# Optimization experiments

Measured on AMD Instinct MI355X. Metric: run time of the kernel, lower is better.

Reference implementation:

```python
import jax, jax.numpy as jnp
import numpy as np

N = 50000      # nodes
E = 800000     # edges (avg degree 16)
IN = 128       # input feature dim
H = 128        # hidden dim (all layers output H; out_channels unused in source)
DROP_P = 0.5


def setup_inputs() -> dict:
    key = jax.random.key(0)
    ks = jax.random.split(key, 8)
    s_in = 1.0 / np.sqrt(IN).astype(np.float32)
    s_h = 1.0 / np.sqrt(H).astype(np.float32)
    return {
        "x": jax.random.normal(ks[0], (N, IN), jnp.float32),
        "edge_index": jax.random.randint(ks[1], (2, E), 0, N, dtype=jnp.int32),
        "Wl0": jax.random.normal(ks[2], (H, IN), jnp.float32) * s_in,
        "bl0": jnp.zeros((H,), jnp.float32),
        "Wr0": jax.random.normal(ks[3], (H, IN), jnp.float32) * s_in,
        "Wl1": jax.random.normal(ks[4], (H, H), jnp.float32) * s_h,
        "bl1": jnp.zeros((H,), jnp.float32),
        "Wr1": jax.random.normal(ks[5], (H, H), jnp.float32) * s_h,
    }


def _sage_conv(x, src, dst, Wl, bl, Wr):
    # mean-aggregate neighbor messages: gather x[src], scatter-add to dst
    agg = jax.ops.segment_sum(x[src], dst, num_segments=N)          # [N, D]
    deg = jax.ops.segment_sum(jnp.ones((src.shape[0],), x.dtype), dst,
                              num_segments=N)                        # [N]
    agg = agg / jnp.maximum(deg, 1.0)[:, None]                       # scatter_mean (0 for isolated nodes)
    # PyG SAGEConv: lin_l(agg) (with bias) + lin_r(x) (no bias)
    return agg @ Wl.T + bl + x @ Wr.T


def reference(x, edge_index, Wl0, bl0, Wr0, Wl1, bl1, Wr1):
    src, dst = edge_index[0], edge_index[1]
    h = _sage_conv(x, src, dst, Wl0, bl0, Wr0)
    h = jax.nn.relu(h)
    # dropout(p=0.5, training=True) with a fixed key for determinism
    keep = jax.random.bernoulli(jax.random.key(42), 1.0 - DROP_P, h.shape)
    h = jnp.where(keep, h / (1.0 - DROP_P), 0.0)
    out = _sage_conv(h, src, dst, Wl1, bl1, Wr1)
    return out
```

## Files before the change

### kernel.cpp

```cpp
#include <hip/hip_runtime.h>
#include <hip/hip_bf16.h>


#define HDIM 128
#define KDIM 256
#define NBUK 256
#define BNODE 196
#define BCAP 4096
#define BCH 2048

typedef __attribute__((ext_vector_type(8))) short bshort8;
typedef __attribute__((ext_vector_type(4))) float f32x4;
typedef __attribute__((ext_vector_type(2))) float f32x2;

__device__ __forceinline__ ushort f2b(float f) {
  __hip_bfloat16 h = __float2bfloat16(f);
  return *(ushort*)&h;
}
__device__ __forceinline__ unsigned int pack2(float lo, float hi) {
  return (unsigned int)f2b(lo) | ((unsigned int)f2b(hi) << 16);
}

#if __has_builtin(__builtin_amdgcn_cvt_pk_f32_fp8) && __has_builtin(__builtin_amdgcn_cvt_pk_fp8_f32)
#define FP8_HW 1
#endif

__device__ __forceinline__ unsigned int fp8e1(float f) {
  unsigned int u = __float_as_uint(f);
  unsigned int s = (u >> 24) & 0x80u;
  unsigned int mag = u & 0x7FFFFFFFu;
  if (mag < 0x38800000u) return s;
  if (mag > 0x43E00000u) mag = 0x43E00000u;
  unsigned int r = mag + 0x7FFFFu + ((mag >> 20) & 1u);
  return s | ((r >> 20) - 960u);
}
__device__ __forceinline__ float fp8d1(unsigned int b) {
  unsigned int v = b & 0x7Fu;
  float fn = __uint_as_float(((b & 0x80u) << 24) | ((v + 960u) << 20));
  return v >= 8u ? fn : 0.0f;
}

__device__ __forceinline__ unsigned int fp8x4_enc(float f0, float f1, float f2, float f3) {
#ifdef FP8_HW
  int u = 0;
  u = __builtin_amdgcn_cvt_pk_fp8_f32(f0, f1, u, false);
  u = __builtin_amdgcn_cvt_pk_fp8_f32(f2, f3, u, true);
  return (unsigned int)u;
#else
  return fp8e1(f0) | (fp8e1(f1) << 8) | (fp8e1(f2) << 16) | (fp8e1(f3) << 24);
#endif
}
__device__ __forceinline__ void fp8x4_acc(float* a, unsigned int w) {
#ifdef FP8_HW
  f32x2 lo = __builtin_amdgcn_cvt_pk_f32_fp8((int)w, false);
  f32x2 hi = __builtin_amdgcn_cvt_pk_f32_fp8((int)w, true);
  a[0] += lo.x; a[1] += lo.y; a[2] += hi.x; a[3] += hi.y;
#else
  a[0] += fp8d1(w & 255u); a[1] += fp8d1((w >> 8) & 255u);
  a[2] += fp8d1((w >> 16) & 255u); a[3] += fp8d1(w >> 24);
#endif
}

__device__ __forceinline__ unsigned int tf_rotl(unsigned int x, int d) {
  return (x << d) | (x >> (32 - d));
}
__device__ __forceinline__ bool dropout_keep(unsigned int j) {
  unsigned int x0 = 0u, x1 = j;
  const unsigned int ks0 = 0u, ks1 = 42u, ks2 = 0x1BD11BDAu ^ 0u ^ 42u;
  x0 += ks0; x1 += ks1;
#define TF_R(r) { x0 += x1; x1 = tf_rotl(x1, (r)); x1 ^= x0; }
  TF_R(13) TF_R(15) TF_R(26) TF_R(6)
  x0 += ks1; x1 += ks2 + 1u;
  TF_R(17) TF_R(29) TF_R(16) TF_R(24)
  x0 += ks2; x1 += ks0 + 2u;
  TF_R(13) TF_R(15) TF_R(26) TF_R(6)
  x0 += ks0; x1 += ks1 + 3u;
  TF_R(17) TF_R(29) TF_R(16) TF_R(24)
  x0 += ks1; x1 += ks2 + 4u;
  TF_R(13) TF_R(15) TF_R(26) TF_R(6)
  x0 += ks2; x1 += ks0 + 5u;
#undef TF_R
  unsigned int r = x0 ^ x1;
  float u = __uint_as_float((r >> 9) | 0x3f800000u) - 1.0f;
  return u < 0.5f;
}

__global__ __launch_bounds__(256) void bin_cvt_k(
    const int* __restrict__ src, const int* __restrict__ dst,
    int* __restrict__ bucketCount, unsigned int* __restrict__ pairs, int E, int EB,
    const float* __restrict__ x,
    const float* __restrict__ Wl0, const float* __restrict__ Wr0,
    const float* __restrict__ Wl1, const float* __restrict__ Wr1,
    ushort* __restrict__ Xb, unsigned char* __restrict__ Xq,
    ushort* __restrict__ Wc0, ushort* __restrict__ Wc1, int N) {
  __shared__ int hist[NBUK];
  __shared__ int lofs[NBUK];
  __shared__ int lcur[NBUK];
  __shared__ int gbase[NBUK];
  __shared__ unsigned int ordv[BCH];
  __shared__ unsigned char ordb[BCH];

  int b = blockIdx.x;
  if (b >= EB) {
    b -= EB;
    if (b < 64) {
      int t = b * 256 + threadIdx.x;
      int o = t >> 7, k = t & 127;
      Wc0[o * KDIM + k] = f2b(Wl0[t]);
      Wc0[o * KDIM + HDIM + k] = f2b(Wr0[t]);
      Wc1[o * KDIM + k] = f2b(Wl1[t]);
      Wc1[o * KDIM + HDIM + k] = f2b(Wr1[t]);
    } else {
      int t = (b - 64) * 256 + threadIdx.x;
      if (t < N * 32) {
        int n = t >> 5, c4 = t & 31;
        float4 v = *(const float4*)&x[(size_t)n * HDIM + c4 * 4];
        uint2 p;
        p.x = pack2(v.x, v.y);
        p.y = pack2(v.z, v.w);
        *(uint2*)&Xb[(size_t)n * HDIM + c4 * 4] = p;
        *(unsigned int*)&Xq[(size_t)n * HDIM + c4 * 4] = fp8x4_enc(v.x, v.y, v.z, v.w);
      }
    }
    return;
  }

  hist[threadIdx.x] = 0;
  __syncthreads();
  int begin = b * BCH;
  int n = min(BCH, E - begin);
  unsigned int vals[BCH / 256];
  int bks[BCH / 256];
  int cnt = 0;
  for (int i = threadIdx.x; i < n; i += 256) {
    int s = src[begin + i], d = dst[begin + i];
    int bk = d / BNODE;
    int dloc = d - bk * BNODE;
    vals[cnt] = ((unsigned int)s << 8) | (unsigned int)dloc;
    bks[cnt] = bk;
    ++cnt;
    atomicAdd(&hist[bk], 1);
  }
  __syncthreads();
  {
    int v = hist[threadIdx.x];
    lofs[threadIdx.x] = v;
    __syncthreads();
    for (int off = 1; off < NBUK; off <<= 1) {
      int t = (threadIdx.x >= off) ? lofs[threadIdx.x - off] : 0;
      __syncthreads();
      lofs[threadIdx.x] += t;
      __syncthreads();
    }
    int ex = lofs[threadIdx.x] - v;
    __syncthreads();
    lofs[threadIdx.x] = ex;
    lcur[threadIdx.x] = ex;
    gbase[threadIdx.x] = atomicAdd(&bucketCount[threadIdx.x], v);
  }
  __syncthreads();
  for (int k = 0; k < cnt; ++k) {
    int bk = bks[k];
    int p = atomicAdd(&lcur[bk], 1);
    ordv[p] = vals[k];
    ordb[p] = (unsigned char)bk;
  }
  __syncthreads();
  for (int j = threadIdx.x; j < n; j += 256) {
    int bk = ordb[j];
    pairs[bk * BCAP + gbase[bk] + (j - lofs[bk])] = ordv[j];
  }
}

__global__ __launch_bounds__(256) void build_k(const unsigned int* __restrict__ pairs,
                                               const int* __restrict__ bucketCount,
                                               int* __restrict__ deg,
                                               int* __restrict__ rowptr,
                                               ushort* __restrict__ eidx, int N) {
  __shared__ int h[BNODE];
  __shared__ int lofs[BNODE];
  __shared__ int cur[BNODE];
  const int b = blockIdx.x;
  const int base = b * BCAP;
  const int cnt = bucketCount[b];
  const int nodebase = b * BNODE;
  const int nloc = min(BNODE, N - nodebase);
  if (threadIdx.x < BNODE) h[threadIdx.x] = 0;
  __syncthreads();
  for (int i = threadIdx.x; i < cnt; i += 256) atomicAdd(&h[pairs[base + i] & 255u], 1);
  __syncthreads();
  if (threadIdx.x < BNODE) lofs[threadIdx.x] = h[threadIdx.x];
  __syncthreads();
  for (int off = 1; off < BNODE; off <<= 1) {
    int t = (threadIdx.x >= off && threadIdx.x < BNODE) ? lofs[threadIdx.x - off] : 0;
    __syncthreads();
    if (threadIdx.x < BNODE) lofs[threadIdx.x] += t;
    __syncthreads();
  }
  if (threadIdx.x < BNODE) {
    int ex = lofs[threadIdx.x] - h[threadIdx.x];
    cur[threadIdx.x] = ex;
    if (threadIdx.x < nloc) {
      deg[nodebase + threadIdx.x] = h[threadIdx.x];
      rowptr[nodebase + threadIdx.x] = base + ex;
    }
  }
  __syncthreads();
  for (int i = threadIdx.x; i < cnt; i += 256) {
    unsigned int v = pairs[base + i];
    int pos = atomicAdd(&cur[v & 255u], 1);
    eidx[base + pos] = (ushort)(v >> 8);
  }
}

__global__ __launch_bounds__(256) void agg_p(const unsigned char* __restrict__ Fq,
                                             ushort* __restrict__ Ag,
                                             const ushort* __restrict__ eidx,
                                             const int* __restrict__ rowptr,
                                             const int* __restrict__ deg, int N) {
  const int lane = threadIdx.x & 63;
  const int wv = threadIdx.x >> 6;
  const int n0 = (blockIdx.x * 4 + wv) * 2;
  if (n0 >= N) return;
  const int n1 = n0 + 1;
  const bool has1 = n1 < N;
  const int es = lane >> 3;
  const int cl = lane & 7;
  const int r0 = rowptr[n0];
  const int d0 = deg[n0];
  const int r1 = has1 ? rowptr[n1] : 0;
  const int d1 = has1 ? deg[n1] : 0;
  float a[16], b[16];
#pragma unroll
  for (int i = 0; i < 16; ++i) { a[i] = 0.0f; b[i] = 0.0f; }
  const int dm = max(d0, d1);
  for (int j = 0; j < dm; j += 16) {
    uint4 va[2], vb[2];
    bool ma[2], mb[2];
#pragma unroll
    for (int u = 0; u < 2; ++u) {
      int e = j + u * 8 + es;
      ma[u] = e < d0;
      mb[u] = e < d1;
      if (ma[u]) {
        int s = eidx[r0 + e];
        va[u] = *(const uint4*)&Fq[(size_t)s * HDIM + cl * 16];
      }
      if (mb[u]) {
        int s = eidx[r1 + e];
        vb[u] = *(const uint4*)&Fq[(size_t)s * HDIM + cl * 16];
      }
    }
#pragma unroll
    for (int u = 0; u < 2; ++u) {
      if (ma[u]) {
        fp8x4_acc(&a[0], va[u].x);
        fp8x4_acc(&a[4], va[u].y);
        fp8x4_acc(&a[8], va[u].z);
        fp8x4_acc(&a[12], va[u].w);
      }
      if (mb[u]) {
        fp8x4_acc(&b[0], vb[u].x);
        fp8x4_acc(&b[4], vb[u].y);
        fp8x4_acc(&b[8], vb[u].z);
        fp8x4_acc(&b[12], vb[u].w);
      }
    }
  }
#pragma unroll
  for (int i = 0; i < 16; ++i) {
    a[i] += __shfl_xor(a[i], 8, 64);
    a[i] += __shfl_xor(a[i], 16, 64);
    a[i] += __shfl_xor(a[i], 32, 64);
    b[i] += __shfl_xor(b[i], 8, 64);
    b[i] += __shfl_xor(b[i], 16, 64);
    b[i] += __shfl_xor(b[i], 32, 64);
  }
  if (es == 0) {
    float rd = 1.0f / fmaxf((float)d0, 1.0f);
    uint4 p0, p1;
    p0.x = pack2(a[0] * rd, a[1] * rd);
    p0.y = pack2(a[2] * rd, a[3] * rd);
    p0.z = pack2(a[4] * rd, a[5] * rd);
    p0.w = pack2(a[6] * rd, a[7] * rd);
    p1.x = pack2(a[8] * rd, a[9] * rd);
    p1.y = pack2(a[10] * rd, a[11] * rd);
    p1.z = pack2(a[12] * rd, a[13] * rd);
    p1.w = pack2(a[14] * rd, a[15] * rd);
    *(uint4*)&Ag[(size_t)n0 * HDIM + cl * 16] = p0;
    *(uint4*)&Ag[(size_t)n0 * HDIM + cl * 16 + 8] = p1;
  } else if (es == 1 && has1) {
    float rd = 1.0f / fmaxf((float)d1, 1.0f);
    uint4 p0, p1;
    p0.x = pack2(b[0] * rd, b[1] * rd);
    p0.y = pack2(b[2] * rd, b[3] * rd);
    p0.z = pack2(b[4] * rd, b[5] * rd);
    p0.w = pack2(b[6] * rd, b[7] * rd);
    p1.x = pack2(b[8] * rd, b[9] * rd);
    p1.y = pack2(b[10] * rd, b[11] * rd);
    p1.z = pack2(b[12] * rd, b[13] * rd);
    p1.w = pack2(b[14] * rd, b[15] * rd);
    *(uint4*)&Ag[(size_t)n1 * HDIM + cl * 16] = p0;
    *(uint4*)&Ag[(size_t)n1 * HDIM + cl * 16 + 8] = p1;
  }
}

template <int MODE>
__global__ __launch_bounds__(256) void gemm_mfma(const ushort* __restrict__ Agg,
                                                 const ushort* __restrict__ F,
                                                 const ushort* __restrict__ Wc,
                                                 ushort* __restrict__ hb,
                                                 unsigned char* __restrict__ hq,
                                                 float* __restrict__ fout,
                                                 const float* __restrict__ bias,
                                                 int N) {
  __shared__ char smem[34816];
  ushort* Wl = (ushort*)smem;
  float* Tl = (float*)smem;
  const int tid = threadIdx.x;
  const int lane = tid & 63;
  const int wid = tid >> 6;
  const int quad = lane >> 4;
  const int l15 = lane & 15;
  const int n0 = blockIdx.x * 64;

  int rowA = n0 + wid * 16 + l15;
  if (rowA >= N) rowA = N - 1;
  bshort8 afA[4], afF[4];
#pragma unroll
  for (int ks = 0; ks < 4; ++ks) {
    afA[ks] = *(const bshort8*)&Agg[(size_t)rowA * HDIM + ks * 32 + quad * 8];
    afF[ks] = *(const bshort8*)&F[(size_t)rowA * HDIM + ks * 32 + quad * 8];
  }

  f32x4 acc[8];
#pragma unroll
  for (int i = 0; i < 8; ++i) acc[i] = (f32x4){0.f, 0.f, 0.f, 0.f};

#pragma unroll
  for (int half = 0; half < 2; ++half) {
    __syncthreads();
#pragma unroll
    for (int i = 0; i < 8; ++i) {
      int q = i * 256 + tid;
      int row = q >> 4, seg = q & 15;
      *(uint4*)&Wl[row * 136 + seg * 8] = *(const uint4*)&Wc[row * KDIM + half * HDIM + seg * 8];
    }
    __syncthreads();
#pragma unroll
    for (int ks = 0; ks < 4; ++ks) {
#pragma unroll
      for (int os = 0; os < 8; ++os) {
        bshort8 bf = *(const bshort8*)&Wl[(os * 16 + l15) * 136 + ks * 32 + quad * 8];
        acc[os] = __builtin_amdgcn_mfma_f32_16x16x32_bf16(
            half == 0 ? afA[ks] : afF[ks], bf, acc[os], 0, 0, 0);
      }
    }
  }

  __syncthreads();

  const int wbase = wid * (16 * 132);
#pragma unroll
  for (int os = 0; os < 8; ++os)
#pragma unroll
    for (int r = 0; r < 4; ++r)
      Tl[wbase + (quad * 4 + r) * 132 + os * 16 + l15] = acc[os][r];

  __syncthreads();

#pragma unroll
  for (int i = 0; i < 8; ++i) {
    int q = i * 64 + lane;
    int r = q >> 5;
    int c4 = q & 31;
    int n = n0 + wid * 16 + r;
    if (n >= N) continue;
    int c = c4 * 4;
    float4 v = *(float4*)&Tl[wbase + r * 132 + c];
    const float4 bv = *(const float4*)&bias[c];
    v.x += bv.x; v.y += bv.y; v.z += bv.z; v.w += bv.w;
    if (MODE == 1) {
      v.x = v.x > 0.0f ? v.x : 0.0f;
      v.y = v.y > 0.0f ? v.y : 0.0f;
      v.z = v.z > 0.0f ? v.z : 0.0f;
      v.w = v.w > 0.0f ? v.w : 0.0f;
      unsigned int fj = (unsigned int)n * HDIM + (unsigned int)c;
      v.x = dropout_keep(fj + 0u) ? v.x * 2.0f : 0.0f;
      v.y = dropout_keep(fj + 1u) ? v.y * 2.0f : 0.0f;
      v.z = dropout_keep(fj + 2u) ? v.z * 2.0f : 0.0f;
      v.w = dropout_keep(fj + 3u) ? v.w * 2.0f : 0.0f;
      uint2 p;
      p.x = pack2(v.x, v.y);
      p.y = pack2(v.z, v.w);
      *(uint2*)&hb[(size_t)n * HDIM + c] = p;
      *(unsigned int*)&hq[(size_t)n * HDIM + c] = fp8x4_enc(v.x, v.y, v.z, v.w);
    } else {
      *(float4*)&fout[(size_t)n * HDIM + c] = v;
    }
  }
}

extern "C" void kernel_launch(void* const* d_in, const int* in_sizes, int n_in,
                              void* d_out, int out_size, void* d_ws, size_t ws_size,
                              hipStream_t stream) {
  const float* x   = (const float*)d_in[0];
  const int*   ei  = (const int*)d_in[1];
  const float* Wl0 = (const float*)d_in[2];
  const float* bl0 = (const float*)d_in[3];
  const float* Wr0 = (const float*)d_in[4];
  const float* Wl1 = (const float*)d_in[5];
  const float* bl1 = (const float*)d_in[6];
  const float* Wr1 = (const float*)d_in[7];
  float* out = (float*)d_out;

  const int N = in_sizes[0] / HDIM;
  const int E = in_sizes[1] / 2;
  const int* src = ei;
  const int* dst = ei + E;

  const int Na = (N + 63) & ~63;
  int* bucketCount = (int*)d_ws;
  int* deg         = bucketCount + NBUK;
  int* rowptr      = deg + Na;
  unsigned int* pairs = (unsigned int*)(rowptr + Na);
  ushort* eidx     = (ushort*)(pairs + NBUK * BCAP);
  size_t off = (((size_t)(eidx + NBUK * BCAP) - (size_t)d_ws) + 255) & ~(size_t)255;
  ushort* Wc0 = (ushort*)((char*)d_ws + off);
  ushort* Wc1 = Wc0 + 128 * KDIM;
  ushort* Xb  = Wc1 + 128 * KDIM;
  ushort* Hb  = Xb + (size_t)N * HDIM;
  ushort* Ag  = Hb + (size_t)N * HDIM;
  unsigned char* Xq = (unsigned char*)(Ag + (size_t)N * HDIM);
  unsigned char* Hq = Xq + (size_t)N * HDIM;

  hipMemsetAsync(bucketCount, 0, NBUK * sizeof(int), stream);

  const int EB = (E + BCH - 1) / BCH;
  const int GB = (N + 63) / 64;
  const int AB = (N + 7) / 8;
  const int CB = EB + 64 + (N * 32 + 255) / 256;

  bin_cvt_k<<<CB, 256, 0, stream>>>(src, dst, bucketCount, pairs, E, EB,
                                    x, Wl0, Wr0, Wl1, Wr1, Xb, Xq, Wc0, Wc1, N);
  build_k<<<NBUK, 256, 0, stream>>>(pairs, bucketCount, deg, rowptr, eidx, N);

  agg_p<<<AB, 256, 0, stream>>>(Xq, Ag, eidx, rowptr, deg, N);
  gemm_mfma<1><<<GB, 256, 0, stream>>>(Ag, Xb, Wc0, Hb, Hq, nullptr, bl0, N);
  agg_p<<<AB, 256, 0, stream>>>(Hq, Ag, eidx, rowptr, deg, N);
  gemm_mfma<2><<<GB, 256, 0, stream>>>(Ag, Hb, Wc1, nullptr, nullptr, out, bl1, N);
}
```

Measured before the change: 216.5 us.

## Fuse neighbor aggregation into the MFMA GEMM kernel via shared memory

Merges the gather-mean aggregation kernel into the GEMM kernel. Each block now aggregates its own 64 nodes into LDS as bf16 and feeds the MFMA directly from there, so the global Ag buffer and two kernel launches go away. In exchange, the grid shrinks from N/8 blocks to N/64, so each wave processes 16 nodes serially. The irregular gather loses parallelism and latency hiding, which may hurt the memory-bound aggregation.

```diff
diff --git a/kernel.cpp b/kernel.cpp
--- a/kernel.cpp
+++ b/kernel.cpp
@@ -213,108 +213,19 @@
   }
 }
 
-__global__ __launch_bounds__(256) void agg_p(const unsigned char* __restrict__ Fq,
-                                             ushort* __restrict__ Ag,
-                                             const ushort* __restrict__ eidx,
-                                             const int* __restrict__ rowptr,
-                                             const int* __restrict__ deg, int N) {
-  const int lane = threadIdx.x & 63;
-  const int wv = threadIdx.x >> 6;
-  const int n0 = (blockIdx.x * 4 + wv) * 2;
-  if (n0 >= N) return;
-  const int n1 = n0 + 1;
-  const bool has1 = n1 < N;
-  const int es = lane >> 3;
-  const int cl = lane & 7;
-  const int r0 = rowptr[n0];
-  const int d0 = deg[n0];
-  const int r1 = has1 ? rowptr[n1] : 0;
-  const int d1 = has1 ? deg[n1] : 0;
-  float a[16], b[16];
-#pragma unroll
-  for (int i = 0; i < 16; ++i) { a[i] = 0.0f; b[i] = 0.0f; }
-  const int dm = max(d0, d1);
-  for (int j = 0; j < dm; j += 16) {
-    uint4 va[2], vb[2];
-    bool ma[2], mb[2];
-#pragma unroll
-    for (int u = 0; u < 2; ++u) {
-      int e = j + u * 8 + es;
-      ma[u] = e < d0;
-      mb[u] = e < d1;
-      if (ma[u]) {
-        int s = eidx[r0 + e];
-        va[u] = *(const uint4*)&Fq[(size_t)s * HDIM + cl * 16];
-      }
-      if (mb[u]) {
-        int s = eidx[r1 + e];
-        vb[u] = *(const uint4*)&Fq[(size_t)s * HDIM + cl * 16];
-      }
-    }
-#pragma unroll
-    for (int u = 0; u < 2; ++u) {
-      if (ma[u]) {
-        fp8x4_acc(&a[0], va[u].x);
-        fp8x4_acc(&a[4], va[u].y);
-        fp8x4_acc(&a[8], va[u].z);
-        fp8x4_acc(&a[12], va[u].w);
-      }
-      if (mb[u]) {
-        fp8x4_acc(&b[0], vb[u].x);
-        fp8x4_acc(&b[4], vb[u].y);
-        fp8x4_acc(&b[8], vb[u].z);
-        fp8x4_acc(&b[12], vb[u].w);
-      }
-    }
-  }
-#pragma unroll
-  for (int i = 0; i < 16; ++i) {
-    a[i] += __shfl_xor(a[i], 8, 64);
-    a[i] += __shfl_xor(a[i], 16, 64);
-    a[i] += __shfl_xor(a[i], 32, 64);
-    b[i] += __shfl_xor(b[i], 8, 64);
-    b[i] += __shfl_xor(b[i], 16, 64);
-    b[i] += __shfl_xor(b[i], 32, 64);
-  }
-  if (es == 0) {
-    float rd = 1.0f / fmaxf((float)d0, 1.0f);
-    uint4 p0, p1;
-    p0.x = pack2(a[0] * rd, a[1] * rd);
-    p0.y = pack2(a[2] * rd, a[3] * rd);
-    p0.z = pack2(a[4] * rd, a[5] * rd);
-    p0.w = pack2(a[6] * rd, a[7] * rd);
-    p1.x = pack2(a[8] * rd, a[9] * rd);
-    p1.y = pack2(a[10] * rd, a[11] * rd);
-    p1.z = pack2(a[12] * rd, a[13] * rd);
-    p1.w = pack2(a[14] * rd, a[15] * rd);
-    *(uint4*)&Ag[(size_t)n0 * HDIM + cl * 16] = p0;
-    *(uint4*)&Ag[(size_t)n0 * HDIM + cl * 16 + 8] = p1;
-  } else if (es == 1 && has1) {
-    float rd = 1.0f / fmaxf((float)d1, 1.0f);
-    uint4 p0, p1;
-    p0.x = pack2(b[0] * rd, b[1] * rd);
-    p0.y = pack2(b[2] * rd, b[3] * rd);
-    p0.z = pack2(b[4] * rd, b[5] * rd);
-    p0.w = pack2(b[6] * rd, b[7] * rd);
-    p1.x = pack2(b[8] * rd, b[9] * rd);
-    p1.y = pack2(b[10] * rd, b[11] * rd);
-    p1.z = pack2(b[12] * rd, b[13] * rd);
-    p1.w = pack2(b[14] * rd, b[15] * rd);
-    *(uint4*)&Ag[(size_t)n1 * HDIM + cl * 16] = p0;
-    *(uint4*)&Ag[(size_t)n1 * HDIM + cl * 16 + 8] = p1;
-  }
-}
-
 template <int MODE>
-__global__ __launch_bounds__(256) void gemm_mfma(const ushort* __restrict__ Agg,
-                                                 const ushort* __restrict__ F,
-                                                 const ushort* __restrict__ Wc,
-                                                 ushort* __restrict__ hb,
-                                                 unsigned char* __restrict__ hq,
-                                                 float* __restrict__ fout,
-                                                 const float* __restrict__ bias,
-                                                 int N) {
+__global__ __launch_bounds__(256) void fused_k(const unsigned char* __restrict__ Fq,
+                                               const ushort* __restrict__ F,
+                                               const ushort* __restrict__ Wc,
+                                               ushort* __restrict__ hb,
+                                               unsigned char* __restrict__ hq,
+                                               float* __restrict__ fout,
+                                               const float* __restrict__ bias,
+                                               const ushort* __restrict__ eidx,
+                                               const int* __restrict__ rowptr,
+                                               const int* __restrict__ deg, int N) {
   __shared__ char smem[34816];
+  ushort* AgL = (ushort*)smem;
   ushort* Wl = (ushort*)smem;
   float* Tl = (float*)smem;
   const int tid = threadIdx.x;
@@ -324,14 +235,107 @@
   const int l15 = lane & 15;
   const int n0 = blockIdx.x * 64;
 
-  int rowA = n0 + wid * 16 + l15;
-  if (rowA >= N) rowA = N - 1;
+  {
+    const int es = lane >> 3;
+    const int cl = lane & 7;
+    for (int p = 0; p < 16; p += 2) {
+      const int ln0 = wid * 16 + p;
+      const int ln1 = ln0 + 1;
+      const int na = n0 + ln0;
+      const int nb2 = n0 + ln1;
+      const int r0 = (na < N) ? rowptr[na] : 0;
+      const int d0 = (na < N) ? deg[na] : 0;
+      const int r1 = (nb2 < N) ? rowptr[nb2] : 0;
+      const int d1 = (nb2 < N) ? deg[nb2] : 0;
+      float a[16], b[16];
+#pragma unroll
+      for (int i = 0; i < 16; ++i) { a[i] = 0.0f; b[i] = 0.0f; }
+      const int dm = max(d0, d1);
+      for (int j = 0; j < dm; j += 16) {
+        uint4 va[2], vb[2];
+        bool ma[2], mb[2];
+#pragma unroll
+        for (int u = 0; u < 2; ++u) {
+          int e = j + u * 8 + es;
+          ma[u] = e < d0;
+          mb[u] = e < d1;
+          if (ma[u]) {
+            int s = eidx[r0 + e];
+            va[u] = *(const uint4*)&Fq[(size_t)s * HDIM + cl * 16];
+          }
+          if (mb[u]) {
+            int s = eidx[r1 + e];
+            vb[u] = *(const uint4*)&Fq[(size_t)s * HDIM + cl * 16];
+          }
+        }
+#pragma unroll
+        for (int u = 0; u < 2; ++u) {
+          if (ma[u]) {
+            fp8x4_acc(&a[0], va[u].x);
+            fp8x4_acc(&a[4], va[u].y);
+            fp8x4_acc(&a[8], va[u].z);
+            fp8x4_acc(&a[12], va[u].w);
+          }
+          if (mb[u]) {
+            fp8x4_acc(&b[0], vb[u].x);
+            fp8x4_acc(&b[4], vb[u].y);
+            fp8x4_acc(&b[8], vb[u].z);
+            fp8x4_acc(&b[12], vb[u].w);
+          }
+        }
+      }
+#pragma unroll
+      for (int i = 0; i < 16; ++i) {
+        a[i] += __shfl_xor(a[i], 8, 64);
+        a[i] += __shfl_xor(a[i], 16, 64);
+        a[i] += __shfl_xor(a[i], 32, 64);
+        b[i] += __shfl_xor(b[i], 8, 64);
+        b[i] += __shfl_xor(b[i], 16, 64);
+        b[i] += __shfl_xor(b[i], 32, 64);
+      }
+      if (es == 0) {
+        float rd = 1.0f / fmaxf((float)d0, 1.0f);
+        uint4 p0, p1;
+        p0.x = pack2(a[0] * rd, a[1] * rd);
+        p0.y = pack2(a[2] * rd, a[3] * rd);
+        p0.z = pack2(a[4] * rd, a[5] * rd);
+        p0.w = pack2(a[6] * rd, a[7] * rd);
+        p1.x = pack2(a[8] * rd, a[9] * rd);
+        p1.y = pack2(a[10] * rd, a[11] * rd);
+        p1.z = pack2(a[12] * rd, a[13] * rd);
+        p1.w = pack2(a[14] * rd, a[15] * rd);
+        *(uint4*)&AgL[ln0 * 136 + cl * 16] = p0;
+        *(uint4*)&AgL[ln0 * 136 + cl * 16 + 8] = p1;
+      } else if (es == 1) {
+        float rd = 1.0f / fmaxf((float)d1, 1.0f);
+        uint4 p0, p1;
+        p0.x = pack2(b[0] * rd, b[1] * rd);
+        p0.y = pack2(b[2] * rd, b[3] * rd);
+        p0.z = pack2(b[4] * rd, b[5] * rd);
+        p0.w = pack2(b[6] * rd, b[7] * rd);
+        p1.x = pack2(b[8] * rd, b[9] * rd);
+        p1.y = pack2(b[10] * rd, b[11] * rd);
+        p1.z = pack2(b[12] * rd, b[13] * rd);
+        p1.w = pack2(b[14] * rd, b[15] * rd);
+        *(uint4*)&AgL[ln1 * 136 + cl * 16] = p0;
+        *(uint4*)&AgL[ln1 * 136 + cl * 16 + 8] = p1;
+      }
+    }
+  }
+  __syncthreads();
+
+  const int lrow = wid * 16 + l15;
   bshort8 afA[4], afF[4];
 #pragma unroll
-  for (int ks = 0; ks < 4; ++ks) {
-    afA[ks] = *(const bshort8*)&Agg[(size_t)rowA * HDIM + ks * 32 + quad * 8];
-    afF[ks] = *(const bshort8*)&F[(size_t)rowA * HDIM + ks * 32 + quad * 8];
-  }
+  for (int ks = 0; ks < 4; ++ks)
+    afA[ks] = *(const bshort8*)&AgL[lrow * 136 + ks * 32 + quad * 8];
+  int rowF = n0 + lrow;
+  if (rowF >= N) rowF = N - 1;
+#pragma unroll
+  for (int ks = 0; ks < 4; ++ks)
+    afF[ks] = *(const bshort8*)&F[(size_t)rowF * HDIM + ks * 32 + quad * 8];
+
+  __syncthreads();
 
   f32x4 acc[8];
 #pragma unroll
@@ -339,7 +343,6 @@
 
 #pragma unroll
   for (int half = 0; half < 2; ++half) {
-    __syncthreads();
 #pragma unroll
     for (int i = 0; i < 8; ++i) {
       int q = i * 256 + tid;
@@ -356,9 +359,8 @@
             half == 0 ? afA[ks] : afF[ks], bf, acc[os], 0, 0, 0);
       }
     }
-  }
-
-  __syncthreads();
+    __syncthreads();
+  }
 
   const int wbase = wid * (16 * 132);
 #pragma unroll
@@ -430,23 +432,21 @@
   ushort* Wc1 = Wc0 + 128 * KDIM;
   ushort* Xb  = Wc1 + 128 * KDIM;
   ushort* Hb  = Xb + (size_t)N * HDIM;
-  ushort* Ag  = Hb + (size_t)N * HDIM;
-  unsigned char* Xq = (unsigned char*)(Ag + (size_t)N * HDIM);
+  unsigned char* Xq = (unsigned char*)(Hb + (size_t)N * HDIM);
   unsigned char* Hq = Xq + (size_t)N * HDIM;
 
   hipMemsetAsync(bucketCount, 0, NBUK * sizeof(int), stream);
 
   const int EB = (E + BCH - 1) / BCH;
   const int GB = (N + 63) / 64;
-  const int AB = (N + 7) / 8;
   const int CB = EB + 64 + (N * 32 + 255) / 256;
 
   bin_cvt_k<<<CB, 256, 0, stream>>>(src, dst, bucketCount, pairs, E, EB,
                                     x, Wl0, Wr0, Wl1, Wr1, Xb, Xq, Wc0, Wc1, N);
   build_k<<<NBUK, 256, 0, stream>>>(pairs, bucketCount, deg, rowptr, eidx, N);
 
-  agg_p<<<AB, 256, 0, stream>>>(Xq, Ag, eidx, rowptr, deg, N);
-  gemm_mfma<1><<<GB, 256, 0, stream>>>(Ag, Xb, Wc0, Hb, Hq, nullptr, bl0, N);
-  agg_p<<<AB, 256, 0, stream>>>(Hq, Ag, eidx, rowptr, deg, N);
-  gemm_mfma<2><<<GB, 256, 0, stream>>>(Ag, Hb, Wc1, nullptr, nullptr, out, bl1, N);
-}
+  fused_k<1><<<GB, 256, 0, stream>>>(Xq, Xb, Wc0, Hb, Hq, nullptr, bl0,
+                                     eidx, rowptr, deg, N);
+  fused_k<2><<<GB, 256, 0, stream>>>(Hq, Hb, Wc1, nullptr, nullptr, out, bl1,
+                                     eidx, rowptr, deg, N);
+}
```

New measurement: 264.2 us. 1.22x slower.
